# Optimization experiments

Measured on AMD Instinct MI355X. Metric: run time of the kernel, lower is better.

The kernel has to match this reference:

```python
import jax, jax.numpy as jnp
import numpy as np


def setup_inputs() -> dict:
    key = jax.random.key(0)
    k1, k2 = jax.random.split(key)
    B, D, H, W = 4, 64, 64, 64
    M = 4096
    z = jax.random.normal(k1, (B, D, H, W), dtype=jnp.float32)
    e = jax.random.normal(k2, (M, D), dtype=jnp.float32)
    log_sigma = jnp.zeros((1,), dtype=jnp.float32)
    return {"z": z, "e": e, "log_sigma": log_sigma}


def reference(z, e, log_sigma):
    # z: [B, D, H, W] latents, e: [M, D] codebook, log_sigma: [1] parameter
    T = 1.0  # latent_temp default
    B, D, H, W = z.shape
    zf = jnp.transpose(z, (0, 2, 3, 1)).reshape(-1, D)  # [N, D]
    N = zf.shape[0]
    # squared pairwise distances via ||z||^2 + ||e||^2 - 2 z e^T (avoids [N,M,D] intermediate)
    d2 = (jnp.sum(zf * zf, axis=1)[:, None]
          + jnp.sum(e * e, axis=1)[None, :]
          - 2.0 * zf @ e.T)  # [N, M]
    alpha = -1.0 / (2.0 * jnp.exp(log_sigma[0]) ** 2)
    matrix = alpha * d2 / T  # [N, M]
    lse = jax.nn.logsumexp(matrix, axis=0)  # [M], reduce over N points per code
    # np.log(np.e) == 1.0
    loss = (-jnp.mean(T * lse)
            + 0.5 * D * (2.0 * log_sigma[0] - 1.0)
            + jnp.log(jnp.asarray(N, dtype=jnp.float32)))
    return loss
```

## Files before the change

### kernel.cpp

```cpp
#include <hip/hip_runtime.h>
#include <hip/hip_bf16.h>
#include <math.h>

#define D_   64
#define HW_  4096
#define N_   16384
#define M_   4096

#define BM 128
#define NSPLIT 16
#define NCHUNK (N_ / NSPLIT)
#define NTILES (NCHUNK / 128)

#define AZN_OFF 0
#define AEN_OFF 16384
#define SUM_OFF 20480
#define ZTB_OFF 24576
#define EBF_OFF (24576 + 524288)
#define WS_FLOATS (EBF_OFF + 131072)

#define L2E 1.4426950408889634f
#define LN2 0.6931471805599453

typedef __attribute__((ext_vector_type(8))) short short8;
typedef __attribute__((ext_vector_type(16))) float floatx16;

#if __has_builtin(__builtin_amdgcn_exp2f)
#define EXP2F(x) __builtin_amdgcn_exp2f(x)
#else
#define EXP2F(x) exp2f(x)
#endif

__device__ __forceinline__ unsigned int bf16_rne(float x) {
    unsigned int u = __float_as_uint(x);
    u += 0x7fffu + ((u >> 16) & 1u);
    return u >> 16;
}

__global__ void prep_kernel(const float* __restrict__ z,
                            const float* __restrict__ e,
                            const float* __restrict__ lsp,
                            float* __restrict__ ws) {
    const float ls = lsp[0];
    const float alpha = -0.5f * __expf(-2.f * ls);
    const float anl = alpha * L2E;
    const float c2p = -2.f * alpha * L2E;
    unsigned short* zTb = (unsigned short*)(ws + ZTB_OFF);
    unsigned short* ebf = (unsigned short*)(ws + EBF_OFF);
    const int blk = blockIdx.x, t = threadIdx.x;

    if (blk < 256) {
        __shared__ float lt[64 * 65];
        const int b = blk >> 6, hw0 = (blk & 63) * 64;
        const int n0 = b * HW_ + hw0;
        const float* zb = z + ((size_t)b * D_) * HW_ + hw0;
#pragma unroll
        for (int i = 0; i < 4; ++i) {
            int idx = t + 256 * i;
            int d = idx >> 4, c = (idx & 15) * 4;
            float4 v = *(const float4*)(zb + (size_t)d * HW_ + c);
            float* p = &lt[d * 65 + c];
            p[0] = v.x; p[1] = v.y; p[2] = v.z; p[3] = v.w;
        }
        __syncthreads();
#pragma unroll
        for (int j = 0; j < 2; ++j) {
            int idx = t + 256 * j;
            int nl = idx >> 3, g = idx & 7;
            float v[8]; float s = 0.f;
#pragma unroll
            for (int jj = 0; jj < 8; ++jj) {
                v[jj] = lt[(8 * g + jj) * 65 + nl];
                s = fmaf(v[jj], v[jj], s);
            }
            s += __shfl_xor(s, 1);
            s += __shfl_xor(s, 2);
            s += __shfl_xor(s, 4);
            uint4 pk;
            pk.x = bf16_rne(v[0] * c2p) | (bf16_rne(v[1] * c2p) << 16);
            pk.y = bf16_rne(v[2] * c2p) | (bf16_rne(v[3] * c2p) << 16);
            pk.z = bf16_rne(v[4] * c2p) | (bf16_rne(v[5] * c2p) << 16);
            pk.w = bf16_rne(v[6] * c2p) | (bf16_rne(v[7] * c2p) << 16);
            *(uint4*)(zTb + (size_t)(n0 + nl) * 64 + 8 * g) = pk;
            if (g == 0) ws[AZN_OFF + n0 + nl] = anl * s;
        }
    } else {
        int m = (blk - 256) * 256 + t;
        const float4* ep = (const float4*)(e + (size_t)m * D_);
        float s = 0.f;
        unsigned int pk[32];
#pragma unroll
        for (int k = 0; k < 16; ++k) {
            float4 v = ep[k];
            s += v.x * v.x + v.y * v.y + v.z * v.z + v.w * v.w;
            pk[2 * k]     = bf16_rne(v.x) | (bf16_rne(v.y) << 16);
            pk[2 * k + 1] = bf16_rne(v.z) | (bf16_rne(v.w) << 16);
        }
        uint4* op = (uint4*)(ebf + (size_t)m * 64);
#pragma unroll
        for (int k = 0; k < 8; ++k)
            op[k] = make_uint4(pk[4 * k], pk[4 * k + 1], pk[4 * k + 2], pk[4 * k + 3]);
        ws[AEN_OFF + m] = anl * s;
        ws[SUM_OFF + m] = 0.f;
    }
}

__global__ __launch_bounds__(256, 2) void main_fast(float* __restrict__ ws) {
    __shared__ float lds_red[BM];
    const unsigned short* zTb = (const unsigned short*)(ws + ZTB_OFF);
    const unsigned short* ebf = (const unsigned short*)(ws + EBF_OFF);
    const float* azn = ws + AZN_OFF;
    float* sums = ws + SUM_OFF;

    const int m0 = blockIdx.x * BM;
    const int ns = blockIdx.y;
    const int t = threadIdx.x;
    const int lane = t & 63;
    const int w = t >> 6;
    const int rlo = lane & 31;
    const int kh = lane >> 5;

    short8 bf[4][4];
#pragma unroll
    for (int mt = 0; mt < 4; ++mt) {
        int row = m0 + mt * 32 + rlo;
#pragma unroll
        for (int ks = 0; ks < 4; ++ks)
            bf[mt][ks] = *(const short8*)(ebf + (size_t)row * 64 + (ks * 2 + kh) * 8);
    }

    float sum[4] = {0.f, 0.f, 0.f, 0.f};
    const int nbase = ns * NCHUNK + w * 32;

    short8 afc[4];
    float4 aznc[4];
    {
#pragma unroll
        for (int ks = 0; ks < 4; ++ks)
            afc[ks] = *(const short8*)(zTb + (size_t)(nbase + rlo) * 64 + (ks * 2 + kh) * 8);
        const int r0 = nbase + 4 * kh;
#pragma unroll
        for (int rg = 0; rg < 4; ++rg) aznc[rg] = *(const float4*)(azn + r0 + 8 * rg);
    }

#pragma unroll
    for (int tile = 0; tile < NTILES; ++tile) {
        short8 afn[4];
        float4 aznn[4];
        if (tile + 1 < NTILES) {
            const int nr = nbase + (tile + 1) * 128;
#pragma unroll
            for (int ks = 0; ks < 4; ++ks)
                afn[ks] = *(const short8*)(zTb + (size_t)(nr + rlo) * 64 + (ks * 2 + kh) * 8);
            const int r0 = nr + 4 * kh;
#pragma unroll
            for (int rg = 0; rg < 4; ++rg) aznn[rg] = *(const float4*)(azn + r0 + 8 * rg);
        }

        float azn_r[16];
#pragma unroll
        for (int rg = 0; rg < 4; ++rg) {
            azn_r[rg * 4 + 0] = aznc[rg].x; azn_r[rg * 4 + 1] = aznc[rg].y;
            azn_r[rg * 4 + 2] = aznc[rg].z; azn_r[rg * 4 + 3] = aznc[rg].w;
        }

        floatx16 acc[4];
#pragma unroll
        for (int mt = 0; mt < 4; ++mt)
#pragma unroll
            for (int r = 0; r < 16; ++r)
                acc[mt][r] = azn_r[r];

#pragma unroll
        for (int ks = 0; ks < 4; ++ks)
#pragma unroll
            for (int mt = 0; mt < 4; ++mt)
                acc[mt] = __builtin_amdgcn_mfma_f32_32x32x16_bf16(
                    afc[ks], bf[mt][ks], acc[mt], 0, 0, 0);

#pragma unroll
        for (int mt = 0; mt < 4; ++mt) {
            float s = 0.f;
#pragma unroll
            for (int r = 0; r < 16; ++r) s += EXP2F(acc[mt][r]);
            sum[mt] += s;
        }

#pragma unroll
        for (int ks = 0; ks < 4; ++ks) afc[ks] = afn[ks];
#pragma unroll
        for (int rg = 0; rg < 4; ++rg) aznc[rg] = aznn[rg];
    }

#pragma unroll
    for (int mt = 0; mt < 4; ++mt) sum[mt] += __shfl_down(sum[mt], 32);

    if (t < BM) lds_red[t] = 0.f;
    __syncthreads();
    if (lane < 32) {
#pragma unroll
        for (int mt = 0; mt < 4; ++mt) atomicAdd(&lds_red[mt * 32 + rlo], sum[mt]);
    }
    __syncthreads();
    if (t < BM) atomicAdd(&sums[m0 + t], lds_red[t]);
}

__global__ void finalize_fast(const float* __restrict__ ws,
                              const float* __restrict__ lsp,
                              float* __restrict__ out) {
    __shared__ double red[256];
    const float* sums = ws + SUM_OFF;
    const float* aen = ws + AEN_OFF;
    int t = threadIdx.x;
    double local = 0.0;
#pragma unroll
    for (int j = 0; j < 16; ++j) {
        int m = t + 256 * j;
        local += (double)(aen[m] + log2f(sums[m]));
    }
    red[t] = local;
    __syncthreads();
    for (int off = 128; off > 0; off >>= 1) {
        if (t < off) red[t] += red[t + off];
        __syncthreads();
    }
    if (t == 0) {
        double ls = (double)lsp[0];
        double loss = -(LN2 * red[0] / (double)M_)
                      + 0.5 * (double)D_ * (2.0 * ls - 1.0)
                      + log((double)N_);
        out[0] = (float)loss;
    }
}

extern "C" void kernel_launch(void* const* d_in, const int* in_sizes, int n_in,
                              void* d_out, int out_size, void* d_ws, size_t ws_size,
                              hipStream_t stream) {
    const float* z   = (const float*)d_in[0];
    const float* e   = (const float*)d_in[1];
    const float* lsp = (const float*)d_in[2];
    float* ws  = (float*)d_ws;
    float* out = (float*)d_out;

    hipLaunchKernelGGL(prep_kernel, dim3(272), dim3(256), 0, stream, z, e, lsp, ws);
    hipLaunchKernelGGL(main_fast, dim3(M_ / BM, NSPLIT), dim3(256), 0, stream, ws);
    hipLaunchKernelGGL(finalize_fast, dim3(1), dim3(256), 0, stream, ws, lsp, out);
}
```

Before: 82.46 us.

## Fuse z-prep, main GEMM-exp and finalize into one persistent kernel with grid barrier

The z transpose/bf16 conversion and the finalize reduction move into the main kernel. A global atomic counter acts as a grid-wide barrier between the z-prep phase and the MFMA phase, and a last-block-done counter runs the final logsumexp reduction. The azn values are staged in LDS, and the m-tiles are processed in two halves to cut register pressure, allowing 3 blocks per SM. This removes two kernel launches and their gaps, but depends on all 512 blocks being co-resident for the spin barrier, so it risks deadlock if occupancy falls short.

```diff
diff --git a/kernel.cpp b/kernel.cpp
--- a/kernel.cpp
+++ b/kernel.cpp
@@ -7,17 +7,17 @@
 #define N_   16384
 #define M_   4096
 
-#define BM 128
-#define NSPLIT 16
-#define NCHUNK (N_ / NSPLIT)
-#define NTILES (NCHUNK / 128)
+#define NSPLIT  16
+#define NCHUNK  1024
+#define NTILES  8
+#define NBLOCKS 512
 
 #define AZN_OFF 0
 #define AEN_OFF 16384
 #define SUM_OFF 20480
-#define ZTB_OFF 24576
-#define EBF_OFF (24576 + 524288)
-#define WS_FLOATS (EBF_OFF + 131072)
+#define CNT_OFF 24576
+#define ZTB_OFF 24592
+#define EBF_OFF (24592 + 524288)
 
 #define L2E 1.4426950408889634f
 #define LN2 0.6931471805599453
@@ -37,89 +37,60 @@
     return u >> 16;
 }
 
-__global__ void prep_kernel(const float* __restrict__ z,
-                            const float* __restrict__ e,
-                            const float* __restrict__ lsp,
-                            float* __restrict__ ws) {
+__global__ void prep_e(const float* __restrict__ e,
+                       const float* __restrict__ lsp,
+                       float* __restrict__ ws) {
     const float ls = lsp[0];
     const float alpha = -0.5f * __expf(-2.f * ls);
     const float anl = alpha * L2E;
-    const float c2p = -2.f * alpha * L2E;
-    unsigned short* zTb = (unsigned short*)(ws + ZTB_OFF);
     unsigned short* ebf = (unsigned short*)(ws + EBF_OFF);
-    const int blk = blockIdx.x, t = threadIdx.x;
-
-    if (blk < 256) {
-        __shared__ float lt[64 * 65];
-        const int b = blk >> 6, hw0 = (blk & 63) * 64;
-        const int n0 = b * HW_ + hw0;
-        const float* zb = z + ((size_t)b * D_) * HW_ + hw0;
-#pragma unroll
-        for (int i = 0; i < 4; ++i) {
-            int idx = t + 256 * i;
-            int d = idx >> 4, c = (idx & 15) * 4;
-            float4 v = *(const float4*)(zb + (size_t)d * HW_ + c);
-            float* p = &lt[d * 65 + c];
-            p[0] = v.x; p[1] = v.y; p[2] = v.z; p[3] = v.w;
-        }
-        __syncthreads();
-#pragma unroll
-        for (int j = 0; j < 2; ++j) {
-            int idx = t + 256 * j;
-            int nl = idx >> 3, g = idx & 7;
-            float v[8]; float s = 0.f;
-#pragma unroll
-            for (int jj = 0; jj < 8; ++jj) {
-                v[jj] = lt[(8 * g + jj) * 65 + nl];
-                s = fmaf(v[jj], v[jj], s);
-            }
-            s += __shfl_xor(s, 1);
-            s += __shfl_xor(s, 2);
-            s += __shfl_xor(s, 4);
-            uint4 pk;
-            pk.x = bf16_rne(v[0] * c2p) | (bf16_rne(v[1] * c2p) << 16);
-            pk.y = bf16_rne(v[2] * c2p) | (bf16_rne(v[3] * c2p) << 16);
-            pk.z = bf16_rne(v[4] * c2p) | (bf16_rne(v[5] * c2p) << 16);
-            pk.w = bf16_rne(v[6] * c2p) | (bf16_rne(v[7] * c2p) << 16);
-            *(uint4*)(zTb + (size_t)(n0 + nl) * 64 + 8 * g) = pk;
-            if (g == 0) ws[AZN_OFF + n0 + nl] = anl * s;
-        }
-    } else {
-        int m = (blk - 256) * 256 + t;
-        const float4* ep = (const float4*)(e + (size_t)m * D_);
-        float s = 0.f;
-        unsigned int pk[32];
-#pragma unroll
-        for (int k = 0; k < 16; ++k) {
-            float4 v = ep[k];
-            s += v.x * v.x + v.y * v.y + v.z * v.z + v.w * v.w;
-            pk[2 * k]     = bf16_rne(v.x) | (bf16_rne(v.y) << 16);
-            pk[2 * k + 1] = bf16_rne(v.z) | (bf16_rne(v.w) << 16);
-        }
-        uint4* op = (uint4*)(ebf + (size_t)m * 64);
-#pragma unroll
-        for (int k = 0; k < 8; ++k)
-            op[k] = make_uint4(pk[4 * k], pk[4 * k + 1], pk[4 * k + 2], pk[4 * k + 3]);
-        ws[AEN_OFF + m] = anl * s;
-        ws[SUM_OFF + m] = 0.f;
-    }
-}
-
-__global__ __launch_bounds__(256, 2) void main_fast(float* __restrict__ ws) {
-    __shared__ float lds_red[BM];
-    const unsigned short* zTb = (const unsigned short*)(ws + ZTB_OFF);
-    const unsigned short* ebf = (const unsigned short*)(ws + EBF_OFF);
-    const float* azn = ws + AZN_OFF;
-    float* sums = ws + SUM_OFF;
-
-    const int m0 = blockIdx.x * BM;
-    const int ns = blockIdx.y;
+    int m = blockIdx.x * 256 + threadIdx.x;
+    const float4* ep = (const float4*)(e + (size_t)m * D_);
+    float s = 0.f;
+    unsigned int pk[32];
+#pragma unroll
+    for (int k = 0; k < 16; ++k) {
+        float4 v = ep[k];
+        s += v.x * v.x + v.y * v.y + v.z * v.z + v.w * v.w;
+        pk[2 * k]     = bf16_rne(v.x) | (bf16_rne(v.y) << 16);
+        pk[2 * k + 1] = bf16_rne(v.z) | (bf16_rne(v.w) << 16);
+    }
+    uint4* op = (uint4*)(ebf + (size_t)m * 64);
+#pragma unroll
+    for (int k = 0; k < 8; ++k)
+        op[k] = make_uint4(pk[4 * k], pk[4 * k + 1], pk[4 * k + 2], pk[4 * k + 3]);
+    ws[AEN_OFF + m] = anl * s;
+    ws[SUM_OFF + m] = 0.f;
+    if (blockIdx.x == 0 && threadIdx.x < 2)
+        ((unsigned*)(ws + CNT_OFF))[threadIdx.x] = 0u;
+}
+
+__global__ __launch_bounds__(256, 3) void fused_kernel(
+        const float* __restrict__ z, const float* __restrict__ lsp,
+        float* __restrict__ ws, float* __restrict__ out) {
+    __shared__ float shmem[2112];
+    __shared__ int is_last;
+
     const int t = threadIdx.x;
     const int lane = t & 63;
     const int w = t >> 6;
     const int rlo = lane & 31;
     const int kh = lane >> 5;
-
+    const int bx = (int)blockIdx.x;
+
+    const float ls = lsp[0];
+    const float alpha = -0.5f * __expf(-2.f * ls);
+    const float anl = alpha * L2E;
+    const float c2p = -2.f * alpha * L2E;
+
+    unsigned short* zTb = (unsigned short*)(ws + ZTB_OFF);
+    const unsigned short* ebf = (const unsigned short*)(ws + EBF_OFF);
+    unsigned* cnt = (unsigned*)(ws + CNT_OFF);
+    float* sums = ws + SUM_OFF;
+
+    const int mblk = bx & 31;
+    const int ns = bx >> 5;
+    const int m0 = mblk * 128;
     short8 bf[4][4];
 #pragma unroll
     for (int mt = 0; mt < 4; ++mt) {
@@ -129,107 +100,156 @@
             bf[mt][ks] = *(const short8*)(ebf + (size_t)row * 64 + (ks * 2 + kh) * 8);
     }
 
+    {
+        const int b = bx >> 7, hw0 = (bx & 127) * 32;
+        const int n0 = b * HW_ + hw0;
+        float* lt = shmem;
+#pragma unroll
+        for (int i = 0; i < 2; ++i) {
+            int idx = t + 256 * i;
+            int d = idx >> 3, c = (idx & 7) * 4;
+            float4 v = *(const float4*)(z + ((size_t)(b * D_ + d)) * HW_ + hw0 + c);
+            float* p = &lt[d * 33 + c];
+            p[0] = v.x; p[1] = v.y; p[2] = v.z; p[3] = v.w;
+        }
+        __syncthreads();
+        const int nl = t >> 3, g = t & 7;
+        float v[8]; float s = 0.f;
+#pragma unroll
+        for (int jj = 0; jj < 8; ++jj) {
+            v[jj] = lt[(8 * g + jj) * 33 + nl];
+            s = fmaf(v[jj], v[jj], s);
+        }
+        s += __shfl_xor(s, 1);
+        s += __shfl_xor(s, 2);
+        s += __shfl_xor(s, 4);
+        uint4 pk;
+        pk.x = bf16_rne(v[0] * c2p) | (bf16_rne(v[1] * c2p) << 16);
+        pk.y = bf16_rne(v[2] * c2p) | (bf16_rne(v[3] * c2p) << 16);
+        pk.z = bf16_rne(v[4] * c2p) | (bf16_rne(v[5] * c2p) << 16);
+        pk.w = bf16_rne(v[6] * c2p) | (bf16_rne(v[7] * c2p) << 16);
+        *(uint4*)(zTb + (size_t)(n0 + nl) * 64 + 8 * g) = pk;
+        if (g == 0) ws[AZN_OFF + n0 + nl] = anl * s;
+    }
+
+    __threadfence();
+    __syncthreads();
+    if (t == 0) {
+        __hip_atomic_fetch_add(&cnt[0], 1u, __ATOMIC_ACQ_REL, __HIP_MEMORY_SCOPE_AGENT);
+        while (__hip_atomic_load(&cnt[0], __ATOMIC_ACQUIRE, __HIP_MEMORY_SCOPE_AGENT) < NBLOCKS)
+            __builtin_amdgcn_s_sleep(1);
+    }
+    __syncthreads();
+    __threadfence();
+
+    float* azn_l = shmem;
+    float* red = shmem + 1024;
+    {
+        const float* azn_g = ws + AZN_OFF + ns * NCHUNK;
+        float4 v = *(const float4*)(azn_g + 4 * t);
+        *(float4*)&azn_l[4 * t] = v;
+    }
+    __syncthreads();
+
     float sum[4] = {0.f, 0.f, 0.f, 0.f};
-    const int nbase = ns * NCHUNK + w * 32;
+    const size_t rowbase = (size_t)(ns * NCHUNK + w * 32 + rlo) * 64 + (size_t)kh * 8;
 
     short8 afc[4];
-    float4 aznc[4];
-    {
-#pragma unroll
-        for (int ks = 0; ks < 4; ++ks)
-            afc[ks] = *(const short8*)(zTb + (size_t)(nbase + rlo) * 64 + (ks * 2 + kh) * 8);
-        const int r0 = nbase + 4 * kh;
-#pragma unroll
-        for (int rg = 0; rg < 4; ++rg) aznc[rg] = *(const float4*)(azn + r0 + 8 * rg);
-    }
+#pragma unroll
+    for (int ks = 0; ks < 4; ++ks)
+        afc[ks] = *(const short8*)(zTb + rowbase + ks * 16);
 
 #pragma unroll
     for (int tile = 0; tile < NTILES; ++tile) {
         short8 afn[4];
-        float4 aznn[4];
         if (tile + 1 < NTILES) {
-            const int nr = nbase + (tile + 1) * 128;
+            const size_t rb = rowbase + (size_t)(tile + 1) * 128 * 64;
 #pragma unroll
             for (int ks = 0; ks < 4; ++ks)
-                afn[ks] = *(const short8*)(zTb + (size_t)(nr + rlo) * 64 + (ks * 2 + kh) * 8);
-            const int r0 = nr + 4 * kh;
-#pragma unroll
-            for (int rg = 0; rg < 4; ++rg) aznn[rg] = *(const float4*)(azn + r0 + 8 * rg);
+                afn[ks] = *(const short8*)(zTb + rb + ks * 16);
         }
 
         float azn_r[16];
+        const int abase = w * 32 + tile * 128 + 4 * kh;
 #pragma unroll
         for (int rg = 0; rg < 4; ++rg) {
-            azn_r[rg * 4 + 0] = aznc[rg].x; azn_r[rg * 4 + 1] = aznc[rg].y;
-            azn_r[rg * 4 + 2] = aznc[rg].z; azn_r[rg * 4 + 3] = aznc[rg].w;
-        }
-
-        floatx16 acc[4];
-#pragma unroll
-        for (int mt = 0; mt < 4; ++mt)
-#pragma unroll
-            for (int r = 0; r < 16; ++r)
-                acc[mt][r] = azn_r[r];
-
-#pragma unroll
-        for (int ks = 0; ks < 4; ++ks)
-#pragma unroll
-            for (int mt = 0; mt < 4; ++mt)
-                acc[mt] = __builtin_amdgcn_mfma_f32_32x32x16_bf16(
-                    afc[ks], bf[mt][ks], acc[mt], 0, 0, 0);
-
-#pragma unroll
-        for (int mt = 0; mt < 4; ++mt) {
-            float s = 0.f;
-#pragma unroll
-            for (int r = 0; r < 16; ++r) s += EXP2F(acc[mt][r]);
-            sum[mt] += s;
+            float4 vv = *(const float4*)&azn_l[abase + 8 * rg];
+            azn_r[rg * 4 + 0] = vv.x; azn_r[rg * 4 + 1] = vv.y;
+            azn_r[rg * 4 + 2] = vv.z; azn_r[rg * 4 + 3] = vv.w;
+        }
+
+#pragma unroll
+        for (int p = 0; p < 2; ++p) {
+            floatx16 acc[2];
+#pragma unroll
+            for (int m2 = 0; m2 < 2; ++m2)
+#pragma unroll
+                for (int r = 0; r < 16; ++r)
+                    acc[m2][r] = azn_r[r];
+#pragma unroll
+            for (int ks = 0; ks < 4; ++ks)
+#pragma unroll
+                for (int m2 = 0; m2 < 2; ++m2)
+                    acc[m2] = __builtin_amdgcn_mfma_f32_32x32x16_bf16(
+                        afc[ks], bf[p * 2 + m2][ks], acc[m2], 0, 0, 0);
+#pragma unroll
+            for (int m2 = 0; m2 < 2; ++m2) {
+                float s = 0.f;
+#pragma unroll
+                for (int r = 0; r < 16; ++r) s += EXP2F(acc[m2][r]);
+                sum[p * 2 + m2] += s;
+            }
         }
 
 #pragma unroll
         for (int ks = 0; ks < 4; ++ks) afc[ks] = afn[ks];
-#pragma unroll
-        for (int rg = 0; rg < 4; ++rg) aznc[rg] = aznn[rg];
     }
 
 #pragma unroll
     for (int mt = 0; mt < 4; ++mt) sum[mt] += __shfl_down(sum[mt], 32);
 
-    if (t < BM) lds_red[t] = 0.f;
+    if (t < 128) red[t] = 0.f;
     __syncthreads();
     if (lane < 32) {
 #pragma unroll
-        for (int mt = 0; mt < 4; ++mt) atomicAdd(&lds_red[mt * 32 + rlo], sum[mt]);
-    }
-    __syncthreads();
-    if (t < BM) atomicAdd(&sums[m0 + t], lds_red[t]);
-}
-
-__global__ void finalize_fast(const float* __restrict__ ws,
-                              const float* __restrict__ lsp,
-                              float* __restrict__ out) {
-    __shared__ double red[256];
-    const float* sums = ws + SUM_OFF;
-    const float* aen = ws + AEN_OFF;
-    int t = threadIdx.x;
-    double local = 0.0;
-#pragma unroll
-    for (int j = 0; j < 16; ++j) {
-        int m = t + 256 * j;
-        local += (double)(aen[m] + log2f(sums[m]));
-    }
-    red[t] = local;
-    __syncthreads();
-    for (int off = 128; off > 0; off >>= 1) {
-        if (t < off) red[t] += red[t + off];
+        for (int mt = 0; mt < 4; ++mt) atomicAdd(&red[mt * 32 + rlo], sum[mt]);
+    }
+    __syncthreads();
+    if (t < 128) atomicAdd(&sums[m0 + t], red[t]);
+
+    __threadfence();
+    __syncthreads();
+    if (t == 0) {
+        unsigned old = __hip_atomic_fetch_add(&cnt[1], 1u, __ATOMIC_ACQ_REL,
+                                              __HIP_MEMORY_SCOPE_AGENT);
+        is_last = (old == NBLOCKS - 1);
+    }
+    __syncthreads();
+    if (is_last) {
+        __threadfence();
+        const float* aen = ws + AEN_OFF;
+        double local = 0.0;
+#pragma unroll
+        for (int j = 0; j < 16; ++j) {
+            int m = t + 256 * j;
+            float s = __hip_atomic_load(&sums[m], __ATOMIC_RELAXED,
+                                        __HIP_MEMORY_SCOPE_AGENT);
+            local += (double)(aen[m] + log2f(s));
+        }
+        double* dred = (double*)(shmem + 1280);
+        dred[t] = local;
         __syncthreads();
-    }
-    if (t == 0) {
-        double ls = (double)lsp[0];
-        double loss = -(LN2 * red[0] / (double)M_)
-                      + 0.5 * (double)D_ * (2.0 * ls - 1.0)
-                      + log((double)N_);
-        out[0] = (float)loss;
+        for (int off = 128; off > 0; off >>= 1) {
+            if (t < off) dred[t] += dred[t + off];
+            __syncthreads();
+        }
+        if (t == 0) {
+            double lsd = (double)ls;
+            double loss = -(LN2 * dred[0] / (double)M_)
+                          + 0.5 * (double)D_ * (2.0 * lsd - 1.0)
+                          + log((double)N_);
+            out[0] = (float)loss;
+        }
     }
 }
 
@@ -242,7 +262,7 @@
     float* ws  = (float*)d_ws;
     float* out = (float*)d_out;
 
-    hipLaunchKernelGGL(prep_kernel, dim3(272), dim3(256), 0, stream, z, e, lsp, ws);
-    hipLaunchKernelGGL(main_fast, dim3(M_ / BM, NSPLIT), dim3(256), 0, stream, ws);
-    hipLaunchKernelGGL(finalize_fast, dim3(1), dim3(256), 0, stream, ws, lsp, out);
-}
+    hipLaunchKernelGGL(prep_e, dim3(16), dim3(256), 0, stream, e, lsp, ws);
+    hipLaunchKernelGGL(fused_kernel, dim3(NBLOCKS), dim3(256), 0, stream,
+                       z, lsp, ws, out);
+}
```

Measured after the change: 205.5 us. +149.2%, slower.

## Switch to 16x16x32 MFMA tiles and fuse finalize via last-block counter

Applied to the files above, without the earlier changes.

The main kernel now uses 16x16x32 bf16 MFMAs with eight 16-row code tiles per wave, in place of 32x32x16 tiles. This shrinks the accumulator register footprint and allows launch bounds of 3 blocks per SM. The separate finalize kernel is folded into the main kernel through a global atomic counter, so the last block computes the loss. The sums and counter are zeroed with a memset instead of in prep. This removes one kernel launch but adds a memset node and fence/atomic overhead in every block.

```diff
diff --git a/kernel.cpp b/kernel.cpp
--- a/kernel.cpp
+++ b/kernel.cpp
@@ -7,23 +7,23 @@
 #define N_   16384
 #define M_   4096
 
-#define BM 128
-#define NSPLIT 16
-#define NCHUNK (N_ / NSPLIT)
-#define NTILES (NCHUNK / 128)
+#define NSPLIT  16
+#define NCHUNK  1024
+#define NSTEPS  16
+#define NBLOCKS 512
 
 #define AZN_OFF 0
 #define AEN_OFF 16384
 #define SUM_OFF 20480
-#define ZTB_OFF 24576
-#define EBF_OFF (24576 + 524288)
-#define WS_FLOATS (EBF_OFF + 131072)
+#define CNT_OFF 24576
+#define ZTB_OFF 24584
+#define EBF_OFF (24584 + 524288)
 
 #define L2E 1.4426950408889634f
 #define LN2 0.6931471805599453
 
 typedef __attribute__((ext_vector_type(8))) short short8;
-typedef __attribute__((ext_vector_type(16))) float floatx16;
+typedef __attribute__((ext_vector_type(4))) float floatx4;
 
 #if __has_builtin(__builtin_amdgcn_exp2f)
 #define EXP2F(x) __builtin_amdgcn_exp2f(x)
@@ -101,135 +101,132 @@
         for (int k = 0; k < 8; ++k)
             op[k] = make_uint4(pk[4 * k], pk[4 * k + 1], pk[4 * k + 2], pk[4 * k + 3]);
         ws[AEN_OFF + m] = anl * s;
-        ws[SUM_OFF + m] = 0.f;
-    }
-}
-
-__global__ __launch_bounds__(256, 2) void main_fast(float* __restrict__ ws) {
-    __shared__ float lds_red[BM];
+    }
+}
+
+__global__ __launch_bounds__(256, 3) void main_fast(
+        const float* __restrict__ lsp, float* __restrict__ ws,
+        float* __restrict__ out) {
+    __shared__ float red[128];
+    __shared__ double dred[256];
+    __shared__ int is_last;
+
+    const int t = threadIdx.x;
+    const int lane = t & 63;
+    const int w = t >> 6;
+    const int li = lane & 15;
+    const int q  = lane >> 4;
+    const int mblk = blockIdx.x;
+    const int ns = blockIdx.y;
+    const int m0 = mblk * 128;
+
     const unsigned short* zTb = (const unsigned short*)(ws + ZTB_OFF);
     const unsigned short* ebf = (const unsigned short*)(ws + EBF_OFF);
     const float* azn = ws + AZN_OFF;
     float* sums = ws + SUM_OFF;
-
-    const int m0 = blockIdx.x * BM;
-    const int ns = blockIdx.y;
-    const int t = threadIdx.x;
-    const int lane = t & 63;
-    const int w = t >> 6;
-    const int rlo = lane & 31;
-    const int kh = lane >> 5;
-
-    short8 bf[4][4];
-#pragma unroll
-    for (int mt = 0; mt < 4; ++mt) {
-        int row = m0 + mt * 32 + rlo;
-#pragma unroll
-        for (int ks = 0; ks < 4; ++ks)
-            bf[mt][ks] = *(const short8*)(ebf + (size_t)row * 64 + (ks * 2 + kh) * 8);
-    }
-
-    float sum[4] = {0.f, 0.f, 0.f, 0.f};
-    const int nbase = ns * NCHUNK + w * 32;
-
-    short8 afc[4];
-    float4 aznc[4];
+    unsigned* cnt = (unsigned*)(ws + CNT_OFF);
+
+    short8 bf[8][2];
+#pragma unroll
+    for (int mt = 0; mt < 8; ++mt) {
+        const size_t rb = (size_t)(m0 + mt * 16 + li) * 64 + q * 8;
+#pragma unroll
+        for (int s = 0; s < 2; ++s)
+            bf[mt][s] = *(const short8*)(ebf + rb + s * 32);
+    }
+
+    float sum[8] = {0.f, 0.f, 0.f, 0.f, 0.f, 0.f, 0.f, 0.f};
+    const int nwbase = ns * NCHUNK + w * 16;
+
+    short8 afc[2];
+    floatx4 aznc;
     {
-#pragma unroll
-        for (int ks = 0; ks < 4; ++ks)
-            afc[ks] = *(const short8*)(zTb + (size_t)(nbase + rlo) * 64 + (ks * 2 + kh) * 8);
-        const int r0 = nbase + 4 * kh;
-#pragma unroll
-        for (int rg = 0; rg < 4; ++rg) aznc[rg] = *(const float4*)(azn + r0 + 8 * rg);
-    }
-
-#pragma unroll
-    for (int tile = 0; tile < NTILES; ++tile) {
-        short8 afn[4];
-        float4 aznn[4];
-        if (tile + 1 < NTILES) {
-            const int nr = nbase + (tile + 1) * 128;
-#pragma unroll
-            for (int ks = 0; ks < 4; ++ks)
-                afn[ks] = *(const short8*)(zTb + (size_t)(nr + rlo) * 64 + (ks * 2 + kh) * 8);
-            const int r0 = nr + 4 * kh;
-#pragma unroll
-            for (int rg = 0; rg < 4; ++rg) aznn[rg] = *(const float4*)(azn + r0 + 8 * rg);
-        }
-
-        float azn_r[16];
-#pragma unroll
-        for (int rg = 0; rg < 4; ++rg) {
-            azn_r[rg * 4 + 0] = aznc[rg].x; azn_r[rg * 4 + 1] = aznc[rg].y;
-            azn_r[rg * 4 + 2] = aznc[rg].z; azn_r[rg * 4 + 3] = aznc[rg].w;
-        }
-
-        floatx16 acc[4];
-#pragma unroll
-        for (int mt = 0; mt < 4; ++mt)
-#pragma unroll
-            for (int r = 0; r < 16; ++r)
-                acc[mt][r] = azn_r[r];
-
-#pragma unroll
-        for (int ks = 0; ks < 4; ++ks)
-#pragma unroll
-            for (int mt = 0; mt < 4; ++mt)
-                acc[mt] = __builtin_amdgcn_mfma_f32_32x32x16_bf16(
-                    afc[ks], bf[mt][ks], acc[mt], 0, 0, 0);
-
-#pragma unroll
-        for (int mt = 0; mt < 4; ++mt) {
-            float s = 0.f;
-#pragma unroll
-            for (int r = 0; r < 16; ++r) s += EXP2F(acc[mt][r]);
-            sum[mt] += s;
-        }
-
-#pragma unroll
-        for (int ks = 0; ks < 4; ++ks) afc[ks] = afn[ks];
-#pragma unroll
-        for (int rg = 0; rg < 4; ++rg) aznc[rg] = aznn[rg];
-    }
-
-#pragma unroll
-    for (int mt = 0; mt < 4; ++mt) sum[mt] += __shfl_down(sum[mt], 32);
-
-    if (t < BM) lds_red[t] = 0.f;
-    __syncthreads();
-    if (lane < 32) {
-#pragma unroll
-        for (int mt = 0; mt < 4; ++mt) atomicAdd(&lds_red[mt * 32 + rlo], sum[mt]);
-    }
-    __syncthreads();
-    if (t < BM) atomicAdd(&sums[m0 + t], lds_red[t]);
-}
-
-__global__ void finalize_fast(const float* __restrict__ ws,
-                              const float* __restrict__ lsp,
-                              float* __restrict__ out) {
-    __shared__ double red[256];
-    const float* sums = ws + SUM_OFF;
-    const float* aen = ws + AEN_OFF;
-    int t = threadIdx.x;
-    double local = 0.0;
-#pragma unroll
-    for (int j = 0; j < 16; ++j) {
-        int m = t + 256 * j;
-        local += (double)(aen[m] + log2f(sums[m]));
-    }
-    red[t] = local;
-    __syncthreads();
-    for (int off = 128; off > 0; off >>= 1) {
-        if (t < off) red[t] += red[t + off];
+        const size_t rb = (size_t)(nwbase + li) * 64 + q * 8;
+        afc[0] = *(const short8*)(zTb + rb);
+        afc[1] = *(const short8*)(zTb + rb + 32);
+        aznc = *(const floatx4*)(azn + nwbase + q * 4);
+    }
+
+#pragma unroll
+    for (int step = 0; step < NSTEPS; ++step) {
+        short8 afn[2];
+        floatx4 aznn;
+        if (step + 1 < NSTEPS) {
+            const int nr = nwbase + (step + 1) * 64;
+            const size_t rb = (size_t)(nr + li) * 64 + q * 8;
+            afn[0] = *(const short8*)(zTb + rb);
+            afn[1] = *(const short8*)(zTb + rb + 32);
+            aznn = *(const floatx4*)(azn + nr + q * 4);
+        }
+
+        floatx4 acc[8];
+#pragma unroll
+        for (int mt = 0; mt < 8; ++mt) acc[mt] = aznc;
+
+#pragma unroll
+        for (int s = 0; s < 2; ++s)
+#pragma unroll
+            for (int mt = 0; mt < 8; ++mt)
+                acc[mt] = __builtin_amdgcn_mfma_f32_16x16x32_bf16(
+                    afc[s], bf[mt][s], acc[mt], 0, 0, 0);
+
+#pragma unroll
+        for (int mt = 0; mt < 8; ++mt) {
+            float s0 = EXP2F(acc[mt][0]) + EXP2F(acc[mt][1]);
+            float s1 = EXP2F(acc[mt][2]) + EXP2F(acc[mt][3]);
+            sum[mt] += s0 + s1;
+        }
+
+        afc[0] = afn[0]; afc[1] = afn[1]; aznc = aznn;
+    }
+
+#pragma unroll
+    for (int mt = 0; mt < 8; ++mt) {
+        sum[mt] += __shfl_xor(sum[mt], 16);
+        sum[mt] += __shfl_xor(sum[mt], 32);
+    }
+
+    if (t < 128) red[t] = 0.f;
+    __syncthreads();
+    if (lane < 16) {
+#pragma unroll
+        for (int mt = 0; mt < 8; ++mt) atomicAdd(&red[mt * 16 + li], sum[mt]);
+    }
+    __syncthreads();
+    if (t < 128) atomicAdd(&sums[m0 + t], red[t]);
+
+    __threadfence();
+    __syncthreads();
+    if (t == 0) {
+        unsigned old = __hip_atomic_fetch_add(cnt, 1u, __ATOMIC_ACQ_REL,
+                                              __HIP_MEMORY_SCOPE_AGENT);
+        is_last = (old == NBLOCKS - 1);
+    }
+    __syncthreads();
+    if (is_last) {
+        __threadfence();
+        const float* aenp = ws + AEN_OFF;
+        double local = 0.0;
+#pragma unroll
+        for (int j = 0; j < 16; ++j) {
+            int m = t + 256 * j;
+            float s = __hip_atomic_load(&sums[m], __ATOMIC_RELAXED,
+                                        __HIP_MEMORY_SCOPE_AGENT);
+            local += (double)(aenp[m] + log2f(s));
+        }
+        dred[t] = local;
         __syncthreads();
-    }
-    if (t == 0) {
-        double ls = (double)lsp[0];
-        double loss = -(LN2 * red[0] / (double)M_)
-                      + 0.5 * (double)D_ * (2.0 * ls - 1.0)
-                      + log((double)N_);
-        out[0] = (float)loss;
+        for (int off = 128; off > 0; off >>= 1) {
+            if (t < off) dred[t] += dred[t + off];
+            __syncthreads();
+        }
+        if (t == 0) {
+            double lsd = (double)lsp[0];
+            double loss = -(LN2 * dred[0] / (double)M_)
+                          + 0.5 * (double)D_ * (2.0 * lsd - 1.0)
+                          + log((double)N_);
+            out[0] = (float)loss;
+        }
     }
 }
 
@@ -242,7 +239,9 @@
     float* ws  = (float*)d_ws;
     float* out = (float*)d_out;
 
+    hipMemsetAsync((char*)d_ws + SUM_OFF * sizeof(float), 0,
+                   4096 * sizeof(float) + 32, stream);
     hipLaunchKernelGGL(prep_kernel, dim3(272), dim3(256), 0, stream, z, e, lsp, ws);
-    hipLaunchKernelGGL(main_fast, dim3(M_ / BM, NSPLIT), dim3(256), 0, stream, ws);
-    hipLaunchKernelGGL(finalize_fast, dim3(1), dim3(256), 0, stream, ws, lsp, out);
-}
+    hipLaunchKernelGGL(main_fast, dim3(32, NSPLIT), dim3(256), 0, stream,
+                       lsp, ws, out);
+}
```

New measurement: 122.3 us. 1.48x slower.

## Split N across more blocks and preload all z tiles up front

Applied to the files above, without the earlier changes.

Raises the N split from 16 to 64, so each block handles 2 tiles of 128 points instead of 8 and the grid grows fourfold. All z fragments and norm values for both tiles are loaded into registers before the loop, replacing the rolling software prefetch. This increases parallelism and hides load latency on a short loop. In exchange there are more global atomics into the per-code sums, the codebook fragments are reloaded by more blocks, and register pressure rises.

```diff
diff --git a/kernel.cpp b/kernel.cpp
--- a/kernel.cpp
+++ b/kernel.cpp
@@ -8,16 +8,15 @@
 #define M_   4096
 
 #define BM 128
-#define NSPLIT 16
+#define NSPLIT 64
 #define NCHUNK (N_ / NSPLIT)
-#define NTILES (NCHUNK / 128)
+#define NTILES 2
 
 #define AZN_OFF 0
 #define AEN_OFF 16384
 #define SUM_OFF 20480
 #define ZTB_OFF 24576
 #define EBF_OFF (24576 + 524288)
-#define WS_FLOATS (EBF_OFF + 131072)
 
 #define L2E 1.4426950408889634f
 #define LN2 0.6931471805599453
@@ -120,6 +119,23 @@
     const int rlo = lane & 31;
     const int kh = lane >> 5;
 
+    const int nbase = ns * NCHUNK + w * 32;
+
+    short8 af[NTILES][4];
+    float4 aznv[NTILES][4];
+#pragma unroll
+    for (int tile = 0; tile < NTILES; ++tile) {
+        const int nr = nbase + tile * 128;
+        const size_t rb = (size_t)(nr + rlo) * 64 + (size_t)kh * 8;
+#pragma unroll
+        for (int ks = 0; ks < 4; ++ks)
+            af[tile][ks] = *(const short8*)(zTb + rb + ks * 16);
+        const int r0 = nr + 4 * kh;
+#pragma unroll
+        for (int rg = 0; rg < 4; ++rg)
+            aznv[tile][rg] = *(const float4*)(azn + r0 + 8 * rg);
+    }
+
     short8 bf[4][4];
 #pragma unroll
     for (int mt = 0; mt < 4; ++mt) {
@@ -130,38 +146,16 @@
     }
 
     float sum[4] = {0.f, 0.f, 0.f, 0.f};
-    const int nbase = ns * NCHUNK + w * 32;
-
-    short8 afc[4];
-    float4 aznc[4];
-    {
-#pragma unroll
-        for (int ks = 0; ks < 4; ++ks)
-            afc[ks] = *(const short8*)(zTb + (size_t)(nbase + rlo) * 64 + (ks * 2 + kh) * 8);
-        const int r0 = nbase + 4 * kh;
-#pragma unroll
-        for (int rg = 0; rg < 4; ++rg) aznc[rg] = *(const float4*)(azn + r0 + 8 * rg);
-    }
 
 #pragma unroll
     for (int tile = 0; tile < NTILES; ++tile) {
-        short8 afn[4];
-        float4 aznn[4];
-        if (tile + 1 < NTILES) {
-            const int nr = nbase + (tile + 1) * 128;
-#pragma unroll
-            for (int ks = 0; ks < 4; ++ks)
-                afn[ks] = *(const short8*)(zTb + (size_t)(nr + rlo) * 64 + (ks * 2 + kh) * 8);
-            const int r0 = nr + 4 * kh;
-#pragma unroll
-            for (int rg = 0; rg < 4; ++rg) aznn[rg] = *(const float4*)(azn + r0 + 8 * rg);
-        }
-
         float azn_r[16];
 #pragma unroll
         for (int rg = 0; rg < 4; ++rg) {
-            azn_r[rg * 4 + 0] = aznc[rg].x; azn_r[rg * 4 + 1] = aznc[rg].y;
-            azn_r[rg * 4 + 2] = aznc[rg].z; azn_r[rg * 4 + 3] = aznc[rg].w;
+            azn_r[rg * 4 + 0] = aznv[tile][rg].x;
+            azn_r[rg * 4 + 1] = aznv[tile][rg].y;
+            azn_r[rg * 4 + 2] = aznv[tile][rg].z;
+            azn_r[rg * 4 + 3] = aznv[tile][rg].w;
         }
 
         floatx16 acc[4];
@@ -176,7 +170,7 @@
 #pragma unroll
             for (int mt = 0; mt < 4; ++mt)
                 acc[mt] = __builtin_amdgcn_mfma_f32_32x32x16_bf16(
-                    afc[ks], bf[mt][ks], acc[mt], 0, 0, 0);
+                    af[tile][ks], bf[mt][ks], acc[mt], 0, 0, 0);
 
 #pragma unroll
         for (int mt = 0; mt < 4; ++mt) {
@@ -185,11 +179,6 @@
             for (int r = 0; r < 16; ++r) s += EXP2F(acc[mt][r]);
             sum[mt] += s;
         }
-
-#pragma unroll
-        for (int ks = 0; ks < 4; ++ks) afc[ks] = afn[ks];
-#pragma unroll
-        for (int rg = 0; rg < 4; ++rg) aznc[rg] = aznn[rg];
     }
 
 #pragma unroll
```

After: 93.21 us. 13.0% more time.
